# Optimization experiments

Measured on AMD Instinct MI355X. Metric: run time of the kernel, lower is better.

## Reference

```python
import jax, jax.numpy as jnp
import numpy as np

IN_DIM = 128
HID = 128
NUM_CLASSES = 10
N_NODES = 100000
N_EDGES = 1600000
NUM_GRAPHS = 128


def setup_inputs() -> dict:
    key = jax.random.key(0)
    ks = jax.random.split(key, 12)
    X = jax.random.normal(ks[0], (N_NODES, IN_DIM), dtype=jnp.float32)
    EI = jax.random.randint(ks[1], (2, N_EDGES), 0, N_NODES, dtype=jnp.int64)
    batch = jnp.sort(jax.random.randint(ks[2], (N_NODES,), 0, NUM_GRAPHS, dtype=jnp.int64))
    s_in = 1.0 / np.sqrt(IN_DIM)
    s_h = 1.0 / np.sqrt(HID)
    s_m = 1.0 / np.sqrt(2 * HID)
    params = {
        'W1': jax.random.uniform(ks[3], (IN_DIM, HID), jnp.float32, -s_in, s_in),
        'b1': jnp.zeros((HID,), jnp.float32),
        'W2': jax.random.uniform(ks[4], (HID, HID), jnp.float32, -s_h, s_h),
        'b2': jnp.zeros((HID,), jnp.float32),
        'W3': jax.random.uniform(ks[5], (HID, HID), jnp.float32, -s_h, s_h),
        'b3': jnp.zeros((HID,), jnp.float32),
        'Wm1': jax.random.uniform(ks[6], (2 * HID, HID), jnp.float32, -s_m, s_m),
        'bm1': jnp.zeros((HID,), jnp.float32),
        'Wm2': jax.random.uniform(ks[7], (HID, NUM_CLASSES), jnp.float32, -s_h, s_h),
        'bm2': jnp.zeros((NUM_CLASSES,), jnp.float32),
    }
    return dict(X=X, EI=EI, batch=batch, num_graphs=NUM_GRAPHS, **params)


def _gcn_norm(EI, n):
    # add self loops, compute D^{-1/2}[row] * D^{-1/2}[col]
    loops = jnp.arange(n, dtype=EI.dtype)
    row = jnp.concatenate([EI[0], loops])
    col = jnp.concatenate([EI[1], loops])
    deg = jax.ops.segment_sum(jnp.ones_like(row, dtype=jnp.float32), row, num_segments=n)
    dis = (deg + 1e-12) ** -0.5
    norm = dis[row] * dis[col]
    return row, col, norm


def _gcn_layer(x, row, col, norm, W, b):
    h = x @ W + b                       # [N, out]
    msg = h[col] * norm[:, None]        # gather + scale  [E+N, out]
    return jax.ops.segment_sum(msg, row, num_segments=x.shape[0])  # scatter-add


def _pool_mean_max(x, batch, num_graphs):
    s = jax.ops.segment_sum(x, batch, num_segments=num_graphs)
    cnt = jax.ops.segment_sum(jnp.ones((x.shape[0],), x.dtype), batch, num_segments=num_graphs)
    mean = s / (cnt[:, None] + 1e-12)
    mx = jax.ops.segment_max(x, batch, num_segments=num_graphs)
    return jnp.concatenate([mean, mx], axis=1)


def reference(X, EI, batch, num_graphs, W1, b1, W2, b2, W3, b3, Wm1, bm1, Wm2, bm2):
    n = X.shape[0]
    row, col, norm = _gcn_norm(EI, n)
    x = jax.nn.relu(_gcn_layer(X, row, col, norm, W1, b1))
    x = jax.nn.relu(_gcn_layer(x, row, col, norm, W2, b2))
    x = jax.nn.relu(_gcn_layer(x, row, col, norm, W3, b3))
    g = _pool_mean_max(x, batch, num_graphs)
    h = jax.nn.relu(g @ Wm1 + bm1)
    return h @ Wm2 + bm2
```

## Files before the change

kernel.cpp:

```cpp
#include <hip/hip_runtime.h>
#include <hip/hip_fp16.h>
#include <cstdint>
#include <cstddef>

#define DIM 128
#define NG 128
#define NCLS 10
#define PSLICE 8
#define CPAD 64
#define NOWN 256
#define RPB 391
#define NPBLK 1024
#define OCAP 16
#define OVCAP 65536

typedef _Float16 f16;
typedef __attribute__((ext_vector_type(8))) _Float16 f16x8;
typedef __attribute__((ext_vector_type(4))) float f32x4;


__global__ __launch_bounds__(256) void k_part(
    const int* __restrict__ rw, const int* __restrict__ cl, int E,
    unsigned long long* __restrict__ buckets, int* __restrict__ bcnt,
    unsigned long long* __restrict__ ovf, int* __restrict__ ovfn) {
  __shared__ int lcnt[NOWN];
  if (threadIdx.x < NOWN) lcnt[threadIdx.x] = 0;
  __syncthreads();
  int b = blockIdx.x;
  int C = (E + NPBLK - 1) / NPBLK;
  int s = b * C;
  int e = s + C;
  if (e > E) e = E;
  for (int i = s + (int)threadIdx.x; i < e; i += 256) {
    int r = rw[i], c = cl[i];
    unsigned long long ent =
        ((unsigned long long)(unsigned)r << 32) | (unsigned)c;
    int o = (unsigned)r / RPB;
    int sl = atomicAdd(&lcnt[o], 1);
    if (sl < OCAP) {
      buckets[((size_t)o * NPBLK + b) * OCAP + sl] = ent;
    } else {
      int oi = atomicAdd(ovfn, 1);
      if (oi < OVCAP) ovf[oi] = ent;
    }
  }
  __syncthreads();
  if (threadIdx.x < NOWN) {
    int v = lcnt[threadIdx.x];
    bcnt[threadIdx.x * NPBLK + b] = v < OCAP ? v : OCAP;
  }
}

__global__ __launch_bounds__(256) void k_place(
    const unsigned long long* __restrict__ buckets, const int* __restrict__ bcnt,
    const unsigned long long* __restrict__ ovf, const int* __restrict__ ovfn,
    int* __restrict__ cnt, int* __restrict__ csrc, int N) {
  extern __shared__ int sm[];
  int* lcnt = sm;
  int* csr = sm + ((RPB + 3) & ~3);
  int o = blockIdx.x;
  int r0 = o * RPB;
  int rows = N - r0;
  if (rows > RPB) rows = RPB;
  if (rows <= 0) return;
  for (int i = threadIdx.x; i < rows; i += 256) lcnt[i] = 0;
  __syncthreads();
  const int* bc = bcnt + o * NPBLK;
  const unsigned long long* bp = buckets + (size_t)o * NPBLK * OCAP;
  for (int j = (int)threadIdx.x; j < NPBLK * OCAP; j += 256) {
    int seg = j >> 4;
    int pos = j & 15;
    if (pos < bc[seg]) {
      unsigned long long ent = bp[j];
      int r = (int)(unsigned)(ent >> 32);
      int c = (int)(unsigned)(ent & 0xffffffffu);
      int li = r - r0;
      int sl = atomicAdd(&lcnt[li], 1);
      if (sl < CPAD) csr[(li << 6) + sl] = c;
    }
  }
  int nov = *ovfn;
  if (nov > OVCAP) nov = OVCAP;
  for (int j = (int)threadIdx.x; j < nov; j += 256) {
    unsigned long long ent = ovf[j];
    int r = (int)(unsigned)(ent >> 32);
    int li = r - r0;
    if (li >= 0 && li < rows) {
      int c = (int)(unsigned)(ent & 0xffffffffu);
      int sl = atomicAdd(&lcnt[li], 1);
      if (sl < CPAD) csr[(li << 6) + sl] = c;
    }
  }
  __syncthreads();
  uint4* dst = (uint4*)(csrc + ((size_t)r0 << 6));
  const uint4* src = (const uint4*)csr;
  int n4 = rows * 16;
  for (int j = (int)threadIdx.x; j < n4; j += 256) dst[j] = src[j];
  for (int i = threadIdx.x; i < rows; i += 256) cnt[r0 + i] = lcnt[i];
}

__global__ void k_dis(const int* __restrict__ cnt, float* __restrict__ dis, int N) {
  int i = blockIdx.x * blockDim.x + threadIdx.x;
  if (i < N) {
    float d = (float)(cnt[i] + 1);
    dis[i] = 1.0f / sqrtf(d);
  }
}

__global__ void k_wt(const float* __restrict__ W1, const float* __restrict__ W2,
                     const float* __restrict__ W3, __half* __restrict__ Wt1,
                     __half* __restrict__ Wt2, __half* __restrict__ Wt3) {
  int gi = blockIdx.x * 256 + threadIdx.x;
  int m = gi / (DIM * DIM);
  int i = gi % (DIM * DIM);
  const float* W = (m == 0) ? W1 : (m == 1) ? W2 : W3;
  __half* Wt = (m == 0) ? Wt1 : (m == 1) ? Wt2 : Wt3;
  int k = i >> 7, c = i & 127;
  Wt[(size_t)c * DIM + k] = __float2half(W[(size_t)k * DIM + c]);
}


template <int FP32IN>
__global__ __launch_bounds__(256, 3) void k_gemm(
    const void* __restrict__ Ain, const __half* __restrict__ Wt,
    const float* __restrict__ bias, const float* __restrict__ dis,
    __half* __restrict__ Hh, int N) {
  int t = threadIdx.x;
  int lane = t & 63;
  int wv = t >> 6;
  int l15 = lane & 15, lg = lane >> 4;
  int cb = (wv & 1) * 64;

  f16x8 bfr[4][4];
#pragma unroll
  for (int ct = 0; ct < 4; ++ct) {
    int c = cb + ct * 16 + l15;
    const f16* wp = (const f16*)Wt + (size_t)c * DIM + lg * 8;
#pragma unroll
    for (int ks = 0; ks < 4; ++ks) bfr[ks][ct] = *(const f16x8*)(wp + ks * 32);
  }
  float bv[4];
#pragma unroll
  for (int ct = 0; ct < 4; ++ct) bv[ct] = bias[cb + ct * 16 + l15];

  const int nt2 = (N + 31) / 32;
  for (int t2 = blockIdx.x; t2 < nt2; t2 += gridDim.x) {
    int row0 = t2 * 32 + (wv >> 1) * 16;
    int rA = row0 + l15;
    if (rA > N - 1) rA = N - 1;
    f16x8 afr[4];
    if constexpr (FP32IN) {
      const float* ap = (const float*)Ain + (size_t)rA * DIM + lg * 8;
#pragma unroll
      for (int ks = 0; ks < 4; ++ks) {
        float4 v0 = *(const float4*)(ap + ks * 32);
        float4 v1 = *(const float4*)(ap + ks * 32 + 4);
        f16x8 a;
        a[0] = (f16)v0.x; a[1] = (f16)v0.y; a[2] = (f16)v0.z; a[3] = (f16)v0.w;
        a[4] = (f16)v1.x; a[5] = (f16)v1.y; a[6] = (f16)v1.z; a[7] = (f16)v1.w;
        afr[ks] = a;
      }
    } else {
      const f16* ap = (const f16*)Ain + (size_t)rA * DIM + lg * 8;
#pragma unroll
      for (int ks = 0; ks < 4; ++ks) afr[ks] = *(const f16x8*)(ap + ks * 32);
    }

    f32x4 acc[4];
#pragma unroll
    for (int ct = 0; ct < 4; ++ct) acc[ct] = (f32x4){0.f, 0.f, 0.f, 0.f};
#pragma unroll
    for (int ks = 0; ks < 4; ++ks)
#pragma unroll
      for (int ct = 0; ct < 4; ++ct)
        acc[ct] = __builtin_amdgcn_mfma_f32_16x16x32_f16(afr[ks], bfr[ks][ct], acc[ct], 0, 0, 0);

#pragma unroll
    for (int j = 0; j < 4; ++j) {
      int r = row0 + lg * 4 + j;
      if (r < N) {
        float dr = dis[r];
#pragma unroll
        for (int ct = 0; ct < 4; ++ct) {
          float o = (acc[ct][j] + bv[ct]) * dr;
          Hh[(size_t)r * DIM + cb + ct * 16 + l15] = __float2half(o);
        }
      }
    }
  }
}


__global__ __launch_bounds__(256) void k_agg(
    const __half* __restrict__ Hh, __half* __restrict__ Ah,
    const int* __restrict__ csrc, const int* __restrict__ cntA,
    const float* __restrict__ dis, int N) {
  int wid = (int)(((size_t)blockIdx.x * blockDim.x + threadIdx.x) >> 6);
  int lane = threadIdx.x & 63;
  if (wid >= N) return;
  int half = lane >> 5;
  int q = lane & 31;
  int cnt = cntA[wid];
  if (cnt > CPAD) cnt = CPAD;
  float dr = dis[wid];
  const int* cp = csrc + ((size_t)wid << 6);
  float4 a0 = {0.f, 0.f, 0.f, 0.f};
  float4 a1 = {0.f, 0.f, 0.f, 0.f};
  float4 a2 = {0.f, 0.f, 0.f, 0.f};
  float4 a3 = {0.f, 0.f, 0.f, 0.f};
  int i = half;
  for (; i + 6 < cnt; i += 8) {
    int c0 = cp[i], c1 = cp[i + 2], c2 = cp[i + 4], c3 = cp[i + 6];
    uint2 u0 = *(const uint2*)(Hh + (size_t)c0 * DIM + q * 4);
    uint2 u1 = *(const uint2*)(Hh + (size_t)c1 * DIM + q * 4);
    uint2 u2 = *(const uint2*)(Hh + (size_t)c2 * DIM + q * 4);
    uint2 u3 = *(const uint2*)(Hh + (size_t)c3 * DIM + q * 4);
    float2 f;
    f = __half22float2(*reinterpret_cast<__half2*>(&u0.x)); a0.x += f.x; a0.y += f.y;
    f = __half22float2(*reinterpret_cast<__half2*>(&u0.y)); a0.z += f.x; a0.w += f.y;
    f = __half22float2(*reinterpret_cast<__half2*>(&u1.x)); a1.x += f.x; a1.y += f.y;
    f = __half22float2(*reinterpret_cast<__half2*>(&u1.y)); a1.z += f.x; a1.w += f.y;
    f = __half22float2(*reinterpret_cast<__half2*>(&u2.x)); a2.x += f.x; a2.y += f.y;
    f = __half22float2(*reinterpret_cast<__half2*>(&u2.y)); a2.z += f.x; a2.w += f.y;
    f = __half22float2(*reinterpret_cast<__half2*>(&u3.x)); a3.x += f.x; a3.y += f.y;
    f = __half22float2(*reinterpret_cast<__half2*>(&u3.y)); a3.z += f.x; a3.w += f.y;
  }
  for (; i < cnt; i += 2) {
    int c0 = cp[i];
    uint2 u0 = *(const uint2*)(Hh + (size_t)c0 * DIM + q * 4);
    float2 f;
    f = __half22float2(*reinterpret_cast<__half2*>(&u0.x)); a0.x += f.x; a0.y += f.y;
    f = __half22float2(*reinterpret_cast<__half2*>(&u0.y)); a0.z += f.x; a0.w += f.y;
  }
  float ax = (a0.x + a1.x) + (a2.x + a3.x);
  float ay = (a0.y + a1.y) + (a2.y + a3.y);
  float az = (a0.z + a1.z) + (a2.z + a3.z);
  float aw = (a0.w + a1.w) + (a2.w + a3.w);
  ax += __shfl_xor(ax, 32);
  ay += __shfl_xor(ay, 32);
  az += __shfl_xor(az, 32);
  aw += __shfl_xor(aw, 32);
  if (lane < 32) {
    uint2 us = *(const uint2*)(Hh + (size_t)wid * DIM + q * 4);
    float2 s0 = __half22float2(*reinterpret_cast<__half2*>(&us.x));
    float2 s1 = __half22float2(*reinterpret_cast<__half2*>(&us.y));
    float ox = fmaxf(dr * (ax + s0.x), 0.f);
    float oy = fmaxf(dr * (ay + s0.y), 0.f);
    float oz = fmaxf(dr * (az + s1.x), 0.f);
    float ow = fmaxf(dr * (aw + s1.y), 0.f);
    __half2 p0 = __floats2half2_rn(ox, oy);
    __half2 p1 = __floats2half2_rn(oz, ow);
    uint2 u;
    u.x = *(unsigned int*)&p0;
    u.y = *(unsigned int*)&p1;
    *(uint2*)(Ah + (size_t)wid * DIM + q * 4) = u;
  }
}


__global__ void k_bounds(const int* __restrict__ batch, int N, int G,
                         int* __restrict__ starts) {
  int i = blockIdx.x * blockDim.x + threadIdx.x;
  if (i >= N) return;
  int b = batch[i];
  int pb = (i == 0) ? -1 : batch[i - 1];
  for (int g = pb + 1; g <= b; ++g) starts[g] = i;
  if (i == N - 1) {
    for (int g = b + 1; g <= G; ++g) starts[g] = N;
  }
}

__global__ void k_pool1(const __half* __restrict__ A, const int* __restrict__ starts,
                        float* __restrict__ part) {
  int g = blockIdx.x / PSLICE, sl = blockIdx.x % PSLICE;
  int c = threadIdx.x;
  int s = starts[g], e = starts[g + 1];
  int len = e - s;
  int ns = s + (len * sl) / PSLICE;
  int ne = s + (len * (sl + 1)) / PSLICE;
  float sum = 0.f, mx = -INFINITY;
  for (int n = ns; n < ne; ++n) {
    float v = __half2float(A[(size_t)n * DIM + c]);
    sum += v;
    mx = fmaxf(mx, v);
  }
  part[((size_t)(g * PSLICE + sl) * 2 + 0) * DIM + c] = sum;
  part[((size_t)(g * PSLICE + sl) * 2 + 1) * DIM + c] = mx;
}

__global__ void k_pool2(const float* __restrict__ part, const int* __restrict__ starts,
                        float* __restrict__ GF) {
  int g = blockIdx.x;
  int c = threadIdx.x;
  float sum = 0.f, mx = -INFINITY;
  for (int sl = 0; sl < PSLICE; ++sl) {
    sum += part[((size_t)(g * PSLICE + sl) * 2 + 0) * DIM + c];
    mx = fmaxf(mx, part[((size_t)(g * PSLICE + sl) * 2 + 1) * DIM + c]);
  }
  int cntg = starts[g + 1] - starts[g];
  GF[(size_t)g * 256 + c] = sum / ((float)cntg + 1e-12f);
  GF[(size_t)g * 256 + 128 + c] = mx;
}


__global__ void k_mlp1(const float* __restrict__ GF, const float* __restrict__ Wm1,
                       const float* __restrict__ bm1, float* __restrict__ H1) {
  __shared__ float gs[256];
  int g = blockIdx.x, j = threadIdx.x;
  gs[j] = GF[(size_t)g * 256 + j];
  gs[j + 128] = GF[(size_t)g * 256 + 128 + j];
  __syncthreads();
  float acc = bm1[j];
#pragma unroll 8
  for (int k = 0; k < 256; ++k) acc = fmaf(gs[k], Wm1[k * DIM + j], acc);
  H1[(size_t)g * DIM + j] = fmaxf(acc, 0.f);
}

__global__ void k_mlp2(const float* __restrict__ H1, const float* __restrict__ Wm2,
                       const float* __restrict__ bm2, float* __restrict__ out) {
  __shared__ float hs[DIM];
  int g = blockIdx.x, j = threadIdx.x;
  hs[j] = H1[(size_t)g * DIM + j];
  hs[j + 64] = H1[(size_t)g * DIM + j + 64];
  __syncthreads();
  if (j < NCLS) {
    float acc = bm2[j];
#pragma unroll 8
    for (int k = 0; k < DIM; ++k) acc = fmaf(hs[k], Wm2[k * NCLS + j], acc);
    out[(size_t)g * NCLS + j] = acc;
  }
}


static inline size_t al256(size_t x) { return (x + 255) & ~(size_t)255; }

extern "C" void kernel_launch(void* const* d_in, const int* in_sizes, int n_in,
                              void* d_out, int out_size, void* d_ws, size_t ws_size,
                              hipStream_t stream) {
  const float* X = (const float*)d_in[0];
  const int* EI = (const int*)d_in[1];
  const int* batch = (const int*)d_in[2];
  const float* W1 = (const float*)d_in[4];
  const float* b1 = (const float*)d_in[5];
  const float* W2 = (const float*)d_in[6];
  const float* b2 = (const float*)d_in[7];
  const float* W3 = (const float*)d_in[8];
  const float* b3 = (const float*)d_in[9];
  const float* Wm1 = (const float*)d_in[10];
  const float* bm1 = (const float*)d_in[11];
  const float* Wm2 = (const float*)d_in[12];
  const float* bm2 = (const float*)d_in[13];
  float* OUT = (float*)d_out;

  const int N = in_sizes[0] / DIM;
  const int E = in_sizes[1] / 2;
  const int G = NG;

  const int* EI_row = EI;
  const int* EI_col = EI + E;

  char* p = (char*)d_ws;
  size_t off = 0;
  auto take = [&](size_t bytes) { void* r = p + off; off = al256(off + bytes); return r; };

  int* cnt = (int*)take((size_t)N * 4);
  int* bcnt = (int*)take((size_t)NOWN * NPBLK * 4);
  int* ovfn = (int*)take(256);
  unsigned long long* ovf = (unsigned long long*)take((size_t)OVCAP * 8);
  int* starts = (int*)take((size_t)(G + 1) * 4);
  float* dis = (float*)take((size_t)N * 4);
  int* csrc = (int*)take((size_t)N * CPAD * 4);
  unsigned long long* buckets =
      (unsigned long long*)take((size_t)NOWN * NPBLK * OCAP * 8);
  __half* Hh = (__half*)take((size_t)N * DIM * 2);
  __half* Ah = (__half*)take((size_t)N * DIM * 2);
  __half* Wt1 = (__half*)take((size_t)DIM * DIM * 2);
  __half* Wt2 = (__half*)take((size_t)DIM * DIM * 2);
  __half* Wt3 = (__half*)take((size_t)DIM * DIM * 2);
  float* part = (float*)take((size_t)G * PSLICE * 2 * DIM * 4);
  float* GF = (float*)take((size_t)G * 256 * 4);
  float* H1 = (float*)take((size_t)G * DIM * 4);
  (void)ws_size; (void)n_in; (void)out_size;

  hipMemsetAsync(ovfn, 0, 4, stream);

  k_part<<<NPBLK, 256, 0, stream>>>(EI_row, EI_col, E, buckets, bcnt, ovf, ovfn);
  const int placeLds = ((RPB + 3) & ~3) * 4 + RPB * 64 * 4;
  k_place<<<NOWN, 256, placeLds, stream>>>(buckets, bcnt, ovf, ovfn, cnt, csrc, N);
  k_dis<<<(N + 255) / 256, 256, 0, stream>>>(cnt, dis, N);
  k_wt<<<192, 256, 0, stream>>>(W1, W2, W3, Wt1, Wt2, Wt3);

  const int aggBlocks = (int)(((size_t)N * 64 + 255) / 256);

  k_gemm<1><<<512, 256, 0, stream>>>(X, Wt1, b1, dis, Hh, N);
  k_agg<<<aggBlocks, 256, 0, stream>>>(Hh, Ah, csrc, cnt, dis, N);
  k_gemm<0><<<512, 256, 0, stream>>>(Ah, Wt2, b2, dis, Hh, N);
  k_agg<<<aggBlocks, 256, 0, stream>>>(Hh, Ah, csrc, cnt, dis, N);
  k_gemm<0><<<512, 256, 0, stream>>>(Ah, Wt3, b3, dis, Hh, N);
  k_agg<<<aggBlocks, 256, 0, stream>>>(Hh, Ah, csrc, cnt, dis, N);

  k_bounds<<<(N + 255) / 256, 256, 0, stream>>>(batch, N, G, starts);
  k_pool1<<<G * PSLICE, DIM, 0, stream>>>(Ah, starts, part);
  k_pool2<<<G, DIM, 0, stream>>>(part, starts, GF);

  k_mlp1<<<G, DIM, 0, stream>>>(GF, Wm1, bm1, H1);
  k_mlp2<<<G, 64, 0, stream>>>(H1, Wm2, bm2, OUT);
}
```

Measured before the change: 383.4 us.

## Pack bucket entries to 32 bits, fuse degree norm, widen aggregation gathers

Bucket entries are packed into 32 bits (local row index shifted left by 17 bits, ORed with the column), halving partition traffic. The separate degree-normalisation kernel is folded into k_place, removing one launch and one pass over the counts. The aggregation kernel now gives each row 16 lanes with 16-byte loads, so one wave handles 4 rows instead of one row split into two halves. That means fewer, wider gathers and no cross-lane shuffle. The risk is that the 17-bit column field only holds node ids below 131072, and fewer waves in flight per row could reduce latency hiding.

```diff
diff --git a/kernel.cpp b/kernel.cpp
--- a/kernel.cpp
+++ b/kernel.cpp
@@ -21,7 +21,7 @@
 
 __global__ __launch_bounds__(256) void k_part(
     const int* __restrict__ rw, const int* __restrict__ cl, int E,
-    unsigned long long* __restrict__ buckets, int* __restrict__ bcnt,
+    unsigned* __restrict__ buckets, int* __restrict__ bcnt,
     unsigned long long* __restrict__ ovf, int* __restrict__ ovfn) {
   __shared__ int lcnt[NOWN];
   if (threadIdx.x < NOWN) lcnt[threadIdx.x] = 0;
@@ -33,15 +33,16 @@
   if (e > E) e = E;
   for (int i = s + (int)threadIdx.x; i < e; i += 256) {
     int r = rw[i], c = cl[i];
-    unsigned long long ent =
-        ((unsigned long long)(unsigned)r << 32) | (unsigned)c;
     int o = (unsigned)r / RPB;
+    int li = r - o * RPB;
     int sl = atomicAdd(&lcnt[o], 1);
     if (sl < OCAP) {
-      buckets[((size_t)o * NPBLK + b) * OCAP + sl] = ent;
+      buckets[((size_t)o * NPBLK + b) * OCAP + sl] =
+          ((unsigned)li << 17) | (unsigned)c;
     } else {
       int oi = atomicAdd(ovfn, 1);
-      if (oi < OVCAP) ovf[oi] = ent;
+      if (oi < OVCAP)
+        ovf[oi] = ((unsigned long long)(unsigned)r << 32) | (unsigned)c;
     }
   }
   __syncthreads();
@@ -52,9 +53,10 @@
 }
 
 __global__ __launch_bounds__(256) void k_place(
-    const unsigned long long* __restrict__ buckets, const int* __restrict__ bcnt,
+    const unsigned* __restrict__ buckets, const int* __restrict__ bcnt,
     const unsigned long long* __restrict__ ovf, const int* __restrict__ ovfn,
-    int* __restrict__ cnt, int* __restrict__ csrc, int N) {
+    int* __restrict__ cnt, float* __restrict__ dis, int* __restrict__ csrc,
+    int N) {
   extern __shared__ int sm[];
   int* lcnt = sm;
   int* csr = sm + ((RPB + 3) & ~3);
@@ -66,15 +68,14 @@
   for (int i = threadIdx.x; i < rows; i += 256) lcnt[i] = 0;
   __syncthreads();
   const int* bc = bcnt + o * NPBLK;
-  const unsigned long long* bp = buckets + (size_t)o * NPBLK * OCAP;
+  const unsigned* bp = buckets + (size_t)o * NPBLK * OCAP;
   for (int j = (int)threadIdx.x; j < NPBLK * OCAP; j += 256) {
     int seg = j >> 4;
     int pos = j & 15;
     if (pos < bc[seg]) {
-      unsigned long long ent = bp[j];
-      int r = (int)(unsigned)(ent >> 32);
-      int c = (int)(unsigned)(ent & 0xffffffffu);
-      int li = r - r0;
+      unsigned ent = bp[j];
+      int li = (int)(ent >> 17);
+      int c = (int)(ent & 0x1ffffu);
       int sl = atomicAdd(&lcnt[li], 1);
       if (sl < CPAD) csr[(li << 6) + sl] = c;
     }
@@ -96,14 +97,10 @@
   const uint4* src = (const uint4*)csr;
   int n4 = rows * 16;
   for (int j = (int)threadIdx.x; j < n4; j += 256) dst[j] = src[j];
-  for (int i = threadIdx.x; i < rows; i += 256) cnt[r0 + i] = lcnt[i];
-}
-
-__global__ void k_dis(const int* __restrict__ cnt, float* __restrict__ dis, int N) {
-  int i = blockIdx.x * blockDim.x + threadIdx.x;
-  if (i < N) {
-    float d = (float)(cnt[i] + 1);
-    dis[i] = 1.0f / sqrtf(d);
+  for (int i = threadIdx.x; i < rows; i += 256) {
+    int v = lcnt[i];
+    cnt[r0 + i] = v;
+    dis[r0 + i] = rsqrtf((float)(v + 1));
   }
 }
 
@@ -195,66 +192,81 @@
     const __half* __restrict__ Hh, __half* __restrict__ Ah,
     const int* __restrict__ csrc, const int* __restrict__ cntA,
     const float* __restrict__ dis, int N) {
-  int wid = (int)(((size_t)blockIdx.x * blockDim.x + threadIdx.x) >> 6);
+  int wave = (int)(((size_t)blockIdx.x * blockDim.x + threadIdx.x) >> 6);
   int lane = threadIdx.x & 63;
-  if (wid >= N) return;
-  int half = lane >> 5;
-  int q = lane & 31;
-  int cnt = cntA[wid];
+  int g = lane >> 4;
+  int q = lane & 15;
+  int r = wave * 4 + g;
+  if (r >= N) return;
+  int cnt = cntA[r];
   if (cnt > CPAD) cnt = CPAD;
-  float dr = dis[wid];
-  const int* cp = csrc + ((size_t)wid << 6);
-  float4 a0 = {0.f, 0.f, 0.f, 0.f};
-  float4 a1 = {0.f, 0.f, 0.f, 0.f};
-  float4 a2 = {0.f, 0.f, 0.f, 0.f};
-  float4 a3 = {0.f, 0.f, 0.f, 0.f};
-  int i = half;
-  for (; i + 6 < cnt; i += 8) {
-    int c0 = cp[i], c1 = cp[i + 2], c2 = cp[i + 4], c3 = cp[i + 6];
-    uint2 u0 = *(const uint2*)(Hh + (size_t)c0 * DIM + q * 4);
-    uint2 u1 = *(const uint2*)(Hh + (size_t)c1 * DIM + q * 4);
-    uint2 u2 = *(const uint2*)(Hh + (size_t)c2 * DIM + q * 4);
-    uint2 u3 = *(const uint2*)(Hh + (size_t)c3 * DIM + q * 4);
-    float2 f;
-    f = __half22float2(*reinterpret_cast<__half2*>(&u0.x)); a0.x += f.x; a0.y += f.y;
-    f = __half22float2(*reinterpret_cast<__half2*>(&u0.y)); a0.z += f.x; a0.w += f.y;
-    f = __half22float2(*reinterpret_cast<__half2*>(&u1.x)); a1.x += f.x; a1.y += f.y;
-    f = __half22float2(*reinterpret_cast<__half2*>(&u1.y)); a1.z += f.x; a1.w += f.y;
-    f = __half22float2(*reinterpret_cast<__half2*>(&u2.x)); a2.x += f.x; a2.y += f.y;
-    f = __half22float2(*reinterpret_cast<__half2*>(&u2.y)); a2.z += f.x; a2.w += f.y;
-    f = __half22float2(*reinterpret_cast<__half2*>(&u3.x)); a3.x += f.x; a3.y += f.y;
-    f = __half22float2(*reinterpret_cast<__half2*>(&u3.y)); a3.z += f.x; a3.w += f.y;
-  }
-  for (; i < cnt; i += 2) {
+  float dr = dis[r];
+  const int* cp = csrc + ((size_t)r << 6);
+  const f16* hb = (const f16*)Hh + q * 8;
+
+  float4 aA0 = {0,0,0,0}, aA1 = {0,0,0,0};
+  float4 aB0 = {0,0,0,0}, aB1 = {0,0,0,0};
+  float4 aC0 = {0,0,0,0}, aC1 = {0,0,0,0};
+  float4 aD0 = {0,0,0,0}, aD1 = {0,0,0,0};
+
+#define ACC8(u, x0, x1)                                                   \
+  {                                                                       \
+    float2 f_;                                                            \
+    f_ = __half22float2(*reinterpret_cast<const __half2*>(&(u).x));       \
+    x0.x += f_.x; x0.y += f_.y;                                           \
+    f_ = __half22float2(*reinterpret_cast<const __half2*>(&(u).y));       \
+    x0.z += f_.x; x0.w += f_.y;                                           \
+    f_ = __half22float2(*reinterpret_cast<const __half2*>(&(u).z));       \
+    x1.x += f_.x; x1.y += f_.y;                                           \
+    f_ = __half22float2(*reinterpret_cast<const __half2*>(&(u).w));       \
+    x1.z += f_.x; x1.w += f_.y;                                           \
+  }
+
+  int i = 0;
+  for (; i + 3 < cnt; i += 4) {
+    int c0 = cp[i], c1 = cp[i + 1], c2 = cp[i + 2], c3 = cp[i + 3];
+    uint4 u0 = *(const uint4*)(hb + (size_t)c0 * DIM);
+    uint4 u1 = *(const uint4*)(hb + (size_t)c1 * DIM);
+    uint4 u2 = *(const uint4*)(hb + (size_t)c2 * DIM);
+    uint4 u3 = *(const uint4*)(hb + (size_t)c3 * DIM);
+    ACC8(u0, aA0, aA1);
+    ACC8(u1, aB0, aB1);
+    ACC8(u2, aC0, aC1);
+    ACC8(u3, aD0, aD1);
+  }
+  for (; i < cnt; ++i) {
     int c0 = cp[i];
-    uint2 u0 = *(const uint2*)(Hh + (size_t)c0 * DIM + q * 4);
-    float2 f;
-    f = __half22float2(*reinterpret_cast<__half2*>(&u0.x)); a0.x += f.x; a0.y += f.y;
-    f = __half22float2(*reinterpret_cast<__half2*>(&u0.y)); a0.z += f.x; a0.w += f.y;
-  }
-  float ax = (a0.x + a1.x) + (a2.x + a3.x);
-  float ay = (a0.y + a1.y) + (a2.y + a3.y);
-  float az = (a0.z + a1.z) + (a2.z + a3.z);
-  float aw = (a0.w + a1.w) + (a2.w + a3.w);
-  ax += __shfl_xor(ax, 32);
-  ay += __shfl_xor(ay, 32);
-  az += __shfl_xor(az, 32);
-  aw += __shfl_xor(aw, 32);
-  if (lane < 32) {
-    uint2 us = *(const uint2*)(Hh + (size_t)wid * DIM + q * 4);
-    float2 s0 = __half22float2(*reinterpret_cast<__half2*>(&us.x));
-    float2 s1 = __half22float2(*reinterpret_cast<__half2*>(&us.y));
-    float ox = fmaxf(dr * (ax + s0.x), 0.f);
-    float oy = fmaxf(dr * (ay + s0.y), 0.f);
-    float oz = fmaxf(dr * (az + s1.x), 0.f);
-    float ow = fmaxf(dr * (aw + s1.y), 0.f);
-    __half2 p0 = __floats2half2_rn(ox, oy);
-    __half2 p1 = __floats2half2_rn(oz, ow);
-    uint2 u;
-    u.x = *(unsigned int*)&p0;
-    u.y = *(unsigned int*)&p1;
-    *(uint2*)(Ah + (size_t)wid * DIM + q * 4) = u;
-  }
+    uint4 u0 = *(const uint4*)(hb + (size_t)c0 * DIM);
+    ACC8(u0, aA0, aA1);
+  }
+  {
+    uint4 us = *(const uint4*)(hb + (size_t)r * DIM);
+    ACC8(us, aA0, aA1);
+  }
+#undef ACC8
+  float4 s0, s1;
+  s0.x = (aA0.x + aB0.x) + (aC0.x + aD0.x);
+  s0.y = (aA0.y + aB0.y) + (aC0.y + aD0.y);
+  s0.z = (aA0.z + aB0.z) + (aC0.z + aD0.z);
+  s0.w = (aA0.w + aB0.w) + (aC0.w + aD0.w);
+  s1.x = (aA1.x + aB1.x) + (aC1.x + aD1.x);
+  s1.y = (aA1.y + aB1.y) + (aC1.y + aD1.y);
+  s1.z = (aA1.z + aB1.z) + (aC1.z + aD1.z);
+  s1.w = (aA1.w + aB1.w) + (aC1.w + aD1.w);
+  float o0 = fmaxf(dr * s0.x, 0.f), o1 = fmaxf(dr * s0.y, 0.f);
+  float o2 = fmaxf(dr * s0.z, 0.f), o3 = fmaxf(dr * s0.w, 0.f);
+  float o4 = fmaxf(dr * s1.x, 0.f), o5 = fmaxf(dr * s1.y, 0.f);
+  float o6 = fmaxf(dr * s1.z, 0.f), o7 = fmaxf(dr * s1.w, 0.f);
+  __half2 p0 = __floats2half2_rn(o0, o1);
+  __half2 p1 = __floats2half2_rn(o2, o3);
+  __half2 p2 = __floats2half2_rn(o4, o5);
+  __half2 p3 = __floats2half2_rn(o6, o7);
+  uint4 u;
+  u.x = *(unsigned int*)&p0;
+  u.y = *(unsigned int*)&p1;
+  u.z = *(unsigned int*)&p2;
+  u.w = *(unsigned int*)&p3;
+  *(uint4*)((f16*)Ah + (size_t)r * DIM + q * 8) = u;
 }
 
 
@@ -370,8 +382,7 @@
   int* starts = (int*)take((size_t)(G + 1) * 4);
   float* dis = (float*)take((size_t)N * 4);
   int* csrc = (int*)take((size_t)N * CPAD * 4);
-  unsigned long long* buckets =
-      (unsigned long long*)take((size_t)NOWN * NPBLK * OCAP * 8);
+  unsigned* buckets = (unsigned*)take((size_t)NOWN * NPBLK * OCAP * 4);
   __half* Hh = (__half*)take((size_t)N * DIM * 2);
   __half* Ah = (__half*)take((size_t)N * DIM * 2);
   __half* Wt1 = (__half*)take((size_t)DIM * DIM * 2);
@@ -386,11 +397,10 @@
 
   k_part<<<NPBLK, 256, 0, stream>>>(EI_row, EI_col, E, buckets, bcnt, ovf, ovfn);
   const int placeLds = ((RPB + 3) & ~3) * 4 + RPB * 64 * 4;
-  k_place<<<NOWN, 256, placeLds, stream>>>(buckets, bcnt, ovf, ovfn, cnt, csrc, N);
-  k_dis<<<(N + 255) / 256, 256, 0, stream>>>(cnt, dis, N);
+  k_place<<<NOWN, 256, placeLds, stream>>>(buckets, bcnt, ovf, ovfn, cnt, dis, csrc, N);
   k_wt<<<192, 256, 0, stream>>>(W1, W2, W3, Wt1, Wt2, Wt3);
 
-  const int aggBlocks = (int)(((size_t)N * 64 + 255) / 256);
+  const int aggBlocks = (N * 16 + 255) / 256;
 
   k_gemm<1><<<512, 256, 0, stream>>>(X, Wt1, b1, dis, Hh, N);
   k_agg<<<aggBlocks, 256, 0, stream>>>(Hh, Ah, csrc, cnt, dis, N);
```

Measured after the change: 367.7 us. 1.04x faster.
